# Kernel tuning notes

Measured on AMD Instinct MI355X. Metric: run time of the kernel, lower is better.

The kernel has to match this reference:

```python
import jax, jax.numpy as jnp
import numpy as np

E, D, H, N = 8, 1024, 4096, 8192  # experts, model dim, moe intermediate, total tokens


def setup_inputs() -> dict:
    key = jax.random.key(0)
    k0, k1, k2, k3 = jax.random.split(key, 4)
    x = jax.random.normal(k0, (N, D), jnp.float32)
    # PrimeRL layout: w1,w3: [E, H, D]; w2: [E, D, H]
    w1 = jax.random.normal(k1, (E, H, D), jnp.float32) * 0.02
    w2 = jax.random.normal(k2, (E, D, H), jnp.float32) * 0.02
    w3 = jax.random.normal(k3, (E, H, D), jnp.float32) * 0.02
    num_tokens_per_expert = jnp.full((E,), N // E, dtype=jnp.int32)  # balanced, sums to N
    return {"x": x, "w1": w1, "w2": w2, "w3": w3,
            "num_tokens_per_expert": num_tokens_per_expert}


def reference(x, w1, w2, w3, num_tokens_per_expert):
    # grouped MoE FFN: per expert e over its contiguous token block,
    #   h = gelu_tanh(x @ w1[e].T) * (x @ w3[e].T); out = h @ w2[e].T
    # torch path casts to bf16 for the grouped mm, casts output back.
    gs = num_tokens_per_expert.astype(jnp.int32)  # group sizes = offsets via cumsum
    xb = x.astype(jnp.bfloat16)
    w1t = jnp.swapaxes(w1, -2, -1).astype(jnp.bfloat16)  # [E, D, H]
    w2t = jnp.swapaxes(w2, -2, -1).astype(jnp.bfloat16)  # [E, H, D]
    w3t = jnp.swapaxes(w3, -2, -1).astype(jnp.bfloat16)  # [E, D, H]
    g = jax.lax.ragged_dot(xb, w1t, gs)                  # [N, H]
    h = jax.nn.gelu(g, approximate=True) * jax.lax.ragged_dot(xb, w3t, gs)
    out = jax.lax.ragged_dot(h, w2t, gs).astype(x.dtype)  # [N, D]
    return out
```

## Files before the change

kernel.cpp:

```cpp
#include <hip/hip_runtime.h>
#include <hip/hip_bf16.h>

#define E_ 8
#define D_ 1024
#define H_ 4096
#define N_ 8192

typedef __attribute__((ext_vector_type(8))) short bf16x8;
typedef __attribute__((ext_vector_type(4))) float f32x4;
typedef unsigned short u16;

static __device__ __forceinline__ u16 f2bf(float f) {
    unsigned int u = __float_as_uint(f);
    u += 0x7fffu + ((u >> 16) & 1u);
    return (u16)(u >> 16);
}

static __device__ __forceinline__ void st_bf4(u16* p, float4 v) {
    union { u16 u[4]; unsigned long long ll; } t;
    t.u[0] = f2bf(v.x); t.u[1] = f2bf(v.y); t.u[2] = f2bf(v.z); t.u[3] = f2bf(v.w);
    *(unsigned long long*)p = t.ll;
}

static __device__ __forceinline__ float gelu_tanh(float x) {
    float x3 = x * x * x;
    float z = 0.7978845608028654f * (x + 0.044715f * x3);
    float t = 1.0f - 2.0f / (1.0f + __expf(2.0f * z));
    return 0.5f * x * (1.0f + t);
}

static __device__ __forceinline__ int expert_of(const int* __restrict__ ntpe, int row) {
    int acc = 0;
    #pragma unroll
    for (int i = 0; i < E_; ++i) {
        acc += ntpe[i];
        if (row < acc) return i;
    }
    return E_ - 1;
}

#define GLD16(gp, lp) __builtin_amdgcn_global_load_lds( \
    (const __attribute__((address_space(1))) void*)(gp), \
    (__attribute__((address_space(3))) void*)(lp), 16, 0, 0)

#define CVT_XBLK 512
#define CVT_WBLK 2048
#define CVT_NBLK (CVT_XBLK + 3 * CVT_WBLK)

__global__ __launch_bounds__(256) void cvt_all2(
    const float* __restrict__ x, const float* __restrict__ w1,
    const float* __restrict__ w2, const float* __restrict__ w3,
    u16* __restrict__ xb, u16* __restrict__ w1b,
    u16* __restrict__ w2b, u16* __restrict__ w3b)
{
    int b = blockIdx.x;
    const float* src; u16* dst; int n8; int b0; int nb;
    if (b < CVT_XBLK) {
        src = x; dst = xb; n8 = N_ * D_ / 8; b0 = 0; nb = CVT_XBLK;
    } else if (b < CVT_XBLK + CVT_WBLK) {
        src = w1; dst = w1b; n8 = E_ * H_ * D_ / 8; b0 = CVT_XBLK; nb = CVT_WBLK;
    } else if (b < CVT_XBLK + 2 * CVT_WBLK) {
        src = w2; dst = w2b; n8 = E_ * D_ * H_ / 8; b0 = CVT_XBLK + CVT_WBLK; nb = CVT_WBLK;
    } else {
        src = w3; dst = w3b; n8 = E_ * H_ * D_ / 8; b0 = CVT_XBLK + 2 * CVT_WBLK; nb = CVT_WBLK;
    }
    int t = (b - b0) * 256 + threadIdx.x;
    int stride = nb * 256;
    const float4* s4 = (const float4*)src;
    for (int i = t; i < n8; i += stride) {
        float4 a = s4[i * 2];
        float4 c = s4[i * 2 + 1];
        union { u16 u[8]; bf16x8 v; } o;
        o.u[0] = f2bf(a.x); o.u[1] = f2bf(a.y); o.u[2] = f2bf(a.z); o.u[3] = f2bf(a.w);
        o.u[4] = f2bf(c.x); o.u[5] = f2bf(c.y); o.u[6] = f2bf(c.z); o.u[7] = f2bf(c.w);
        *(bf16x8*)(dst + (size_t)i * 8) = o.v;
    }
}


#define EPIT 72

__global__ __launch_bounds__(256, 3) void moe_gemm13_fast(
    const u16* __restrict__ xb, const u16* __restrict__ w1b,
    const u16* __restrict__ w3b, const int* __restrict__ ntpe,
    u16* __restrict__ hbuf)
{
    __shared__ u16 smem[16384];
    u16* sA  = smem;
    u16* sB1 = smem + 8192;
    u16* sB2 = smem + 12288;

    const int tid = threadIdx.x;
    const int m0 = blockIdx.y * 128, n0 = blockIdx.x * 64;
    const int e = expert_of(ntpe, m0);
    const int wave = tid >> 6, lane = tid & 63;
    const int wm = (wave >> 1) * 64, wn = (wave & 1) * 32;
    const int fr = lane & 15, quad = lane >> 4;
    const int sw = fr & 7;

    const u16* Ag  = xb  + (size_t)m0 * D_;
    const u16* B1g = w1b + ((size_t)e * H_ + n0) * D_;
    const u16* B2g = w3b + ((size_t)e * H_ + n0) * D_;

    const int srr = lane >> 3;
    const int scg = ((lane & 7) ^ srr) * 8;

    f32x4 accg[4][2], accu[4][2];
    #pragma unroll
    for (int i = 0; i < 4; ++i)
        #pragma unroll
        for (int j = 0; j < 2; ++j) {
            accg[i][j] = (f32x4){0.f, 0.f, 0.f, 0.f};
            accu[i][j] = (f32x4){0.f, 0.f, 0.f, 0.f};
        }

    for (int k0 = 0; k0 < D_; k0 += 64) {
        #pragma unroll
        for (int c = 0; c < 4; ++c)
            GLD16(Ag + (size_t)(wave * 32 + c * 8 + srr) * D_ + k0 + scg,
                  sA + (wave * 32 + c * 8) * 64);
        #pragma unroll
        for (int c = 0; c < 2; ++c) {
            GLD16(B1g + (size_t)(wave * 16 + c * 8 + srr) * D_ + k0 + scg,
                  sB1 + (wave * 16 + c * 8) * 64);
            GLD16(B2g + (size_t)(wave * 16 + c * 8 + srr) * D_ + k0 + scg,
                  sB2 + (wave * 16 + c * 8) * 64);
        }
        __syncthreads();

        #pragma unroll
        for (int kh = 0; kh < 2; ++kh) {
            const int ks = ((quad + kh * 4) ^ sw) * 8;
            bf16x8 fa[4], fb1[2], fb2[2];
            #pragma unroll
            for (int i = 0; i < 4; ++i)
                fa[i] = *(const bf16x8*)(&sA[(wm + i * 16 + fr) * 64 + ks]);
            #pragma unroll
            for (int j = 0; j < 2; ++j) {
                fb1[j] = *(const bf16x8*)(&sB1[(wn + j * 16 + fr) * 64 + ks]);
                fb2[j] = *(const bf16x8*)(&sB2[(wn + j * 16 + fr) * 64 + ks]);
            }
            #pragma unroll
            for (int i = 0; i < 4; ++i)
                #pragma unroll
                for (int j = 0; j < 2; ++j) {
                    accg[i][j] = __builtin_amdgcn_mfma_f32_16x16x32_bf16(fa[i], fb1[j], accg[i][j], 0, 0, 0);
                    accu[i][j] = __builtin_amdgcn_mfma_f32_16x16x32_bf16(fa[i], fb2[j], accu[i][j], 0, 0, 0);
                }
        }
        __syncthreads();
    }

    #pragma unroll
    for (int i = 0; i < 4; ++i) {
        int rl = wm + i * 16 + quad * 4;
        #pragma unroll
        for (int j = 0; j < 2; ++j) {
            int cl = wn + j * 16 + fr;
            #pragma unroll
            for (int r = 0; r < 4; ++r) {
                float hv = gelu_tanh(accg[i][j][r]) * accu[i][j][r];
                smem[(rl + r) * EPIT + cl] = f2bf(hv);
            }
        }
    }
    __syncthreads();
    #pragma unroll
    for (int it = 0; it < 4; ++it) {
        int chunk = it * 256 + tid;
        int row = chunk >> 3;
        int col = (chunk & 7) * 8;
        bf16x8 v = *(const bf16x8*)(&smem[row * EPIT + col]);
        *(bf16x8*)(&hbuf[(size_t)(m0 + row) * H_ + n0 + col]) = v;
    }
}

__global__ __launch_bounds__(256, 3) void moe_gemm2_fast(
    const u16* __restrict__ hbuf, const u16* __restrict__ w2b,
    const int* __restrict__ ntpe, float* __restrict__ out)
{
    __shared__ u16 smem[16384];
    u16* sA = smem;
    u16* sB = smem + 8192;

    const int tid = threadIdx.x;
    const int m0 = blockIdx.y * 128, n0 = blockIdx.x * 128;
    const int e = expert_of(ntpe, m0);
    const int wave = tid >> 6, lane = tid & 63;
    const int wm = (wave >> 1) * 64, wn = (wave & 1) * 64;
    const int fr = lane & 15, quad = lane >> 4;
    const int sw = fr & 7;

    const u16* Ag = hbuf + (size_t)m0 * H_;
    const u16* Bg = w2b + ((size_t)e * D_ + n0) * H_;

    const int srr = lane >> 3;
    const int scg = ((lane & 7) ^ srr) * 8;

    f32x4 acc[4][4];
    #pragma unroll
    for (int i = 0; i < 4; ++i)
        #pragma unroll
        for (int j = 0; j < 4; ++j)
            acc[i][j] = (f32x4){0.f, 0.f, 0.f, 0.f};

    for (int k0 = 0; k0 < H_; k0 += 64) {
        #pragma unroll
        for (int c = 0; c < 4; ++c) {
            GLD16(Ag + (size_t)(wave * 32 + c * 8 + srr) * H_ + k0 + scg,
                  sA + (wave * 32 + c * 8) * 64);
            GLD16(Bg + (size_t)(wave * 32 + c * 8 + srr) * H_ + k0 + scg,
                  sB + (wave * 32 + c * 8) * 64);
        }
        __syncthreads();

        #pragma unroll
        for (int kh = 0; kh < 2; ++kh) {
            const int ks = ((quad + kh * 4) ^ sw) * 8;
            bf16x8 fa[4], fb[4];
            #pragma unroll
            for (int i = 0; i < 4; ++i) {
                fa[i] = *(const bf16x8*)(&sA[(wm + i * 16 + fr) * 64 + ks]);
                fb[i] = *(const bf16x8*)(&sB[(wn + i * 16 + fr) * 64 + ks]);
            }
            #pragma unroll
            for (int i = 0; i < 4; ++i)
                #pragma unroll
                for (int j = 0; j < 4; ++j)
                    acc[i][j] = __builtin_amdgcn_mfma_f32_16x16x32_bf16(fa[i], fb[j], acc[i][j], 0, 0, 0);
        }
        __syncthreads();
    }

    #pragma unroll
    for (int i = 0; i < 4; ++i) {
        int rowb = m0 + wm + i * 16 + quad * 4;
        #pragma unroll
        for (int j = 0; j < 4; ++j) {
            int col = n0 + wn + j * 16 + fr;
            #pragma unroll
            for (int r = 0; r < 4; ++r)
                out[(size_t)(rowb + r) * D_ + col] = acc[i][j][r];
        }
    }
}

#define LDSP 40

__global__ __launch_bounds__(256, 2) void moe_gemm13_slow(
    const float* __restrict__ x, const float* __restrict__ w1,
    const float* __restrict__ w3, const int* __restrict__ ntpe,
    u16* __restrict__ hbuf)
{
    const int tid = threadIdx.x;
    const int m0 = blockIdx.y * 128, n0 = blockIdx.x * 128;
    const int e = expert_of(ntpe, m0);
    __shared__ u16 sA[128][LDSP]; __shared__ u16 sB1[128][LDSP]; __shared__ u16 sB2[128][LDSP];
    const int wave = tid >> 6, lane = tid & 63;
    const int wm = (wave >> 1) * 64, wn = (wave & 1) * 64;
    const int fr = lane & 15, quad = lane >> 4;
    f32x4 accg[4][4], accu[4][4];
    #pragma unroll
    for (int i = 0; i < 4; ++i)
        #pragma unroll
        for (int j = 0; j < 4; ++j) {
            accg[i][j] = (f32x4){0.f,0.f,0.f,0.f}; accu[i][j] = (f32x4){0.f,0.f,0.f,0.f};
        }
    const float* Ab  = x  + (size_t)m0 * D_;
    const float* B1b = w1 + ((size_t)e * H_ + n0) * D_;
    const float* B2b = w3 + ((size_t)e * H_ + n0) * D_;
    for (int k0 = 0; k0 < D_; k0 += 32) {
        #pragma unroll
        for (int s = 0; s < 4; ++s) {
            int idx = s * 256 + tid;
            int row = idx >> 3, col = (idx & 7) * 4;
            size_t go = (size_t)row * D_ + k0 + col;
            st_bf4(&sA[row][col],  *(const float4*)(Ab + go));
            st_bf4(&sB1[row][col], *(const float4*)(B1b + go));
            st_bf4(&sB2[row][col], *(const float4*)(B2b + go));
        }
        __syncthreads();
        bf16x8 fa[4], fb1[4], fb2[4];
        #pragma unroll
        for (int i = 0; i < 4; ++i) {
            fa[i]  = *(const bf16x8*)(&sA[wm + i * 16 + fr][quad * 8]);
            fb1[i] = *(const bf16x8*)(&sB1[wn + i * 16 + fr][quad * 8]);
            fb2[i] = *(const bf16x8*)(&sB2[wn + i * 16 + fr][quad * 8]);
        }
        #pragma unroll
        for (int i = 0; i < 4; ++i)
            #pragma unroll
            for (int j = 0; j < 4; ++j) {
                accg[i][j] = __builtin_amdgcn_mfma_f32_16x16x32_bf16(fa[i], fb1[j], accg[i][j], 0, 0, 0);
                accu[i][j] = __builtin_amdgcn_mfma_f32_16x16x32_bf16(fa[i], fb2[j], accu[i][j], 0, 0, 0);
            }
        __syncthreads();
    }
    #pragma unroll
    for (int i = 0; i < 4; ++i) {
        int rowb = m0 + wm + i * 16 + quad * 4;
        #pragma unroll
        for (int j = 0; j < 4; ++j) {
            int col = n0 + wn + j * 16 + fr;
            #pragma unroll
            for (int r = 0; r < 4; ++r)
                hbuf[(size_t)(rowb + r) * H_ + col] = f2bf(gelu_tanh(accg[i][j][r]) * accu[i][j][r]);
        }
    }
}

__global__ __launch_bounds__(256, 2) void moe_gemm2_slow(
    const u16* __restrict__ hbuf, const float* __restrict__ w2,
    const int* __restrict__ ntpe, float* __restrict__ out)
{
    const int tid = threadIdx.x;
    const int m0 = blockIdx.y * 128, n0 = blockIdx.x * 128;
    const int e = expert_of(ntpe, m0);
    __shared__ u16 sA[128][LDSP]; __shared__ u16 sB[128][LDSP];
    const int wave = tid >> 6, lane = tid & 63;
    const int wm = (wave >> 1) * 64, wn = (wave & 1) * 64;
    const int fr = lane & 15, quad = lane >> 4;
    f32x4 acc[4][4];
    #pragma unroll
    for (int i = 0; i < 4; ++i)
        #pragma unroll
        for (int j = 0; j < 4; ++j) acc[i][j] = (f32x4){0.f,0.f,0.f,0.f};
    const u16* Ab = hbuf + (size_t)m0 * H_;
    const float* Bb = w2 + ((size_t)e * D_ + n0) * H_;
    for (int k0 = 0; k0 < H_; k0 += 32) {
        #pragma unroll
        for (int s = 0; s < 2; ++s) {
            int idx = s * 256 + tid;
            int row = idx >> 2, col = (idx & 3) * 8;
            *(bf16x8*)(&sA[row][col]) = *(const bf16x8*)(Ab + (size_t)row * H_ + k0 + col);
        }
        #pragma unroll
        for (int s = 0; s < 4; ++s) {
            int idx = s * 256 + tid;
            int row = idx >> 3, col = (idx & 7) * 4;
            st_bf4(&sB[row][col], *(const float4*)(Bb + (size_t)row * H_ + k0 + col));
        }
        __syncthreads();
        bf16x8 fa[4], fb[4];
        #pragma unroll
        for (int i = 0; i < 4; ++i) {
            fa[i] = *(const bf16x8*)(&sA[wm + i * 16 + fr][quad * 8]);
            fb[i] = *(const bf16x8*)(&sB[wn + i * 16 + fr][quad * 8]);
        }
        #pragma unroll
        for (int i = 0; i < 4; ++i)
            #pragma unroll
            for (int j = 0; j < 4; ++j)
                acc[i][j] = __builtin_amdgcn_mfma_f32_16x16x32_bf16(fa[i], fb[j], acc[i][j], 0, 0, 0);
        __syncthreads();
    }
    #pragma unroll
    for (int i = 0; i < 4; ++i) {
        int rowb = m0 + wm + i * 16 + quad * 4;
        #pragma unroll
        for (int j = 0; j < 4; ++j) {
            int col = n0 + wn + j * 16 + fr;
            #pragma unroll
            for (int r = 0; r < 4; ++r)
                out[(size_t)(rowb + r) * D_ + col] = acc[i][j][r];
        }
    }
}

extern "C" void kernel_launch(void* const* d_in, const int* in_sizes, int n_in,
                              void* d_out, int out_size, void* d_ws, size_t ws_size,
                              hipStream_t stream) {
    const float* x  = (const float*)d_in[0];
    const float* w1 = (const float*)d_in[1];
    const float* w2 = (const float*)d_in[2];
    const float* w3 = (const float*)d_in[3];
    const int* ntpe = (const int*)d_in[4];
    float* out = (float*)d_out;

    const size_t SZ_XB = (size_t)N_ * D_ * 2;
    const size_t SZ_W  = (size_t)E_ * H_ * D_ * 2;
    const size_t SZ_H  = (size_t)N_ * H_ * 2;
    const size_t NEED  = SZ_XB + 3 * SZ_W + SZ_H;

    if (ws_size >= NEED) {
        char* p = (char*)d_ws;
        u16* xb  = (u16*)p;                 p += SZ_XB;
        u16* w1b = (u16*)p;                 p += SZ_W;
        u16* w3b = (u16*)p;                 p += SZ_W;
        u16* w2b = (u16*)p;                 p += SZ_W;
        u16* hb  = (u16*)p;

        cvt_all2<<<CVT_NBLK, 256, 0, stream>>>(x, w1, w2, w3, xb, w1b, w2b, w3b);

        dim3 g1(H_ / 64, N_ / 128);
        moe_gemm13_fast<<<g1, 256, 0, stream>>>(xb, w1b, w3b, ntpe, hb);

        dim3 g2(D_ / 128, N_ / 128);
        moe_gemm2_fast<<<g2, 256, 0, stream>>>(hb, w2b, ntpe, out);
    } else {
        u16* hb = (u16*)d_ws;
        dim3 g1(H_ / 128, N_ / 128);
        moe_gemm13_slow<<<g1, 256, 0, stream>>>(x, w1, w3, ntpe, hb);
        dim3 g2(D_ / 128, N_ / 128);
        moe_gemm2_slow<<<g2, 256, 0, stream>>>(hb, w2, ntpe, out);
    }
}
```

Measured before the change: 643.6 us.

## Swizzle GEMM block order for L2/XCD locality and use nontemporal loads/stores

Both GEMM kernels switch to a 1D grid, remapping block IDs so consecutive blocks round-robined across the 8 XCDs share the same expert's M-rows and weight columns. This aims to improve L2 reuse of weight tiles. The conversion kernel is reordered to do w2 first with nontemporal stores and uses nontemporal loads, and the final output store is nontemporal, reducing cache pollution from streaming data. The remap assumes specific grid sizes and an 8-way XCD dispatch.

```diff
diff --git a/kernel.cpp b/kernel.cpp
--- a/kernel.cpp
+++ b/kernel.cpp
@@ -8,6 +8,7 @@
 
 typedef __attribute__((ext_vector_type(8))) short bf16x8;
 typedef __attribute__((ext_vector_type(4))) float f32x4;
+typedef __attribute__((ext_vector_type(4))) float fv4;
 typedef unsigned short u16;
 
 static __device__ __forceinline__ u16 f2bf(float f) {
@@ -54,26 +55,27 @@
     u16* __restrict__ w2b, u16* __restrict__ w3b)
 {
     int b = blockIdx.x;
-    const float* src; u16* dst; int n8; int b0; int nb;
-    if (b < CVT_XBLK) {
-        src = x; dst = xb; n8 = N_ * D_ / 8; b0 = 0; nb = CVT_XBLK;
-    } else if (b < CVT_XBLK + CVT_WBLK) {
-        src = w1; dst = w1b; n8 = E_ * H_ * D_ / 8; b0 = CVT_XBLK; nb = CVT_WBLK;
-    } else if (b < CVT_XBLK + 2 * CVT_WBLK) {
-        src = w2; dst = w2b; n8 = E_ * D_ * H_ / 8; b0 = CVT_XBLK + CVT_WBLK; nb = CVT_WBLK;
+    const float* src; u16* dst; int n8; int b0; int nb; bool nts = false;
+    if (b < CVT_WBLK) {
+        src = w2; dst = w2b; n8 = E_ * D_ * H_ / 8; b0 = 0; nb = CVT_WBLK; nts = true;
+    } else if (b < 2 * CVT_WBLK) {
+        src = w1; dst = w1b; n8 = E_ * H_ * D_ / 8; b0 = CVT_WBLK; nb = CVT_WBLK;
+    } else if (b < 3 * CVT_WBLK) {
+        src = w3; dst = w3b; n8 = E_ * H_ * D_ / 8; b0 = 2 * CVT_WBLK; nb = CVT_WBLK;
     } else {
-        src = w3; dst = w3b; n8 = E_ * H_ * D_ / 8; b0 = CVT_XBLK + 2 * CVT_WBLK; nb = CVT_WBLK;
+        src = x; dst = xb; n8 = N_ * D_ / 8; b0 = 3 * CVT_WBLK; nb = CVT_XBLK;
     }
     int t = (b - b0) * 256 + threadIdx.x;
     int stride = nb * 256;
-    const float4* s4 = (const float4*)src;
+    const fv4* s4 = (const fv4*)src;
     for (int i = t; i < n8; i += stride) {
-        float4 a = s4[i * 2];
-        float4 c = s4[i * 2 + 1];
+        fv4 a = __builtin_nontemporal_load(s4 + (size_t)i * 2);
+        fv4 c = __builtin_nontemporal_load(s4 + (size_t)i * 2 + 1);
         union { u16 u[8]; bf16x8 v; } o;
         o.u[0] = f2bf(a.x); o.u[1] = f2bf(a.y); o.u[2] = f2bf(a.z); o.u[3] = f2bf(a.w);
         o.u[4] = f2bf(c.x); o.u[5] = f2bf(c.y); o.u[6] = f2bf(c.z); o.u[7] = f2bf(c.w);
-        *(bf16x8*)(dst + (size_t)i * 8) = o.v;
+        if (nts) __builtin_nontemporal_store(o.v, (bf16x8*)(dst + (size_t)i * 8));
+        else *(bf16x8*)(dst + (size_t)i * 8) = o.v;
     }
 }
 
@@ -91,7 +93,11 @@
     u16* sB2 = smem + 12288;
 
     const int tid = threadIdx.x;
-    const int m0 = blockIdx.y * 128, n0 = blockIdx.x * 64;
+    const int bswz = (blockIdx.x & 7) * (4096 / 8) + (blockIdx.x >> 3);
+    const int eg = bswz >> 9;
+    const int rr = bswz & 511;
+    const int m0 = (eg * 8 + (rr & 7)) * 128;
+    const int n0 = (rr >> 3) * 64;
     const int e = expert_of(ntpe, m0);
     const int wave = tid >> 6, lane = tid & 63;
     const int wm = (wave >> 1) * 64, wn = (wave & 1) * 32;
@@ -184,7 +190,11 @@
     u16* sB = smem + 8192;
 
     const int tid = threadIdx.x;
-    const int m0 = blockIdx.y * 128, n0 = blockIdx.x * 128;
+    const int bswz = (blockIdx.x & 7) * (512 / 8) + (blockIdx.x >> 3);
+    const int eg = bswz >> 6;
+    const int rr = bswz & 63;
+    const int m0 = (eg * 8 + (rr & 7)) * 128;
+    const int n0 = (rr >> 3) * 128;
     const int e = expert_of(ntpe, m0);
     const int wave = tid >> 6, lane = tid & 63;
     const int wm = (wave >> 1) * 64, wn = (wave & 1) * 64;
@@ -240,7 +250,7 @@
             int col = n0 + wn + j * 16 + fr;
             #pragma unroll
             for (int r = 0; r < 4; ++r)
-                out[(size_t)(rowb + r) * D_ + col] = acc[i][j][r];
+                __builtin_nontemporal_store(acc[i][j][r], &out[(size_t)(rowb + r) * D_ + col]);
         }
     }
 }
@@ -392,11 +402,9 @@
 
         cvt_all2<<<CVT_NBLK, 256, 0, stream>>>(x, w1, w2, w3, xb, w1b, w2b, w3b);
 
-        dim3 g1(H_ / 64, N_ / 128);
-        moe_gemm13_fast<<<g1, 256, 0, stream>>>(xb, w1b, w3b, ntpe, hb);
-
-        dim3 g2(D_ / 128, N_ / 128);
-        moe_gemm2_fast<<<g2, 256, 0, stream>>>(hb, w2b, ntpe, out);
+        moe_gemm13_fast<<<4096, 256, 0, stream>>>(xb, w1b, w3b, ntpe, hb);
+
+        moe_gemm2_fast<<<512, 256, 0, stream>>>(hb, w2b, ntpe, out);
     } else {
         u16* hb = (u16*)d_ws;
         dim3 g1(H_ / 128, N_ / 128);
```

Measured after the change: 618.7 us. 3.9% less time.
